# Optimization experiments

Measured on AMD Instinct MI355X. Metric: run time of the kernel, lower is better.

Reference implementation:

```python
import jax, jax.numpy as jnp
import numpy as np

N_HEAD = 16
LN_EPS = 1e-5

def _layernorm(x, g, b):
    mu = jnp.mean(x, axis=-1, keepdims=True)
    var = jnp.mean(jnp.square(x - mu), axis=-1, keepdims=True)
    return (x - mu) * jax.lax.rsqrt(var + LN_EPS) * g + b

def setup_inputs() -> dict:
    key = jax.random.key(0)
    ks = jax.random.split(key, 8)
    B, T, C, L, V = 4, 512, 1024, 8, 32000
    s = 0.02
    return {
        "idx": jax.random.randint(ks[0], (B, T), 0, V, dtype=jnp.int32),
        "tok_emb": jax.random.normal(ks[1], (V, C), jnp.float32) * s,
        "pos_emb": jax.random.normal(ks[2], (T, C), jnp.float32) * s,
        "ln1_g": jnp.ones((L, C), jnp.float32),
        "ln1_b": jnp.zeros((L, C), jnp.float32),
        "attn_w": jax.random.normal(ks[3], (L, 3 * C, C), jnp.float32) * s,
        "proj_w": jax.random.normal(ks[4], (L, C, C), jnp.float32) * s,
        "ln2_g": jnp.ones((L, C), jnp.float32),
        "ln2_b": jnp.zeros((L, C), jnp.float32),
        "mlp_w1": jax.random.normal(ks[5], (L, 4 * C, C), jnp.float32) * s,
        "mlp_w2": jax.random.normal(ks[6], (L, C, 4 * C), jnp.float32) * s,
        "lnf_g": jnp.ones((C,), jnp.float32),
        "lnf_b": jnp.zeros((C,), jnp.float32),
        "head_w": jax.random.normal(ks[7], (V, C), jnp.float32) * s,
    }

def reference(idx, tok_emb, pos_emb, ln1_g, ln1_b, attn_w, proj_w,
              ln2_g, ln2_b, mlp_w1, mlp_w2, lnf_g, lnf_b, head_w):
    B, T = idx.shape
    C = tok_emb.shape[1]
    H = N_HEAD
    D = C // H
    scale = 1.0 / np.sqrt(D).astype(np.float32)
    x = tok_emb[idx] + pos_emb[:T]            # [B,T,C]
    causal = jnp.tril(jnp.ones((T, T), bool))  # [T,T]

    def block(x, p):
        g1, b1, wqkv, wp, g2, b2, w1, w2 = p
        h = _layernorm(x, g1, b1)
        qkv = h @ wqkv.T                       # [B,T,3C]
        q, k, v = jnp.split(qkv, 3, axis=-1)
        q = q.reshape(B, T, H, D).transpose(0, 2, 1, 3)  # [B,H,T,D]
        k = k.reshape(B, T, H, D).transpose(0, 2, 1, 3)
        v = v.reshape(B, T, H, D).transpose(0, 2, 1, 3)
        att = jnp.einsum('bhqd,bhkd->bhqk', q, k) * scale
        att = jnp.where(causal, att, -jnp.inf)
        att = jax.nn.softmax(att, axis=-1)
        y = jnp.einsum('bhqk,bhkd->bhqd', att, v)
        y = y.transpose(0, 2, 1, 3).reshape(B, T, C)
        a = x + y @ wp.T                       # attn residual (inner)
        m = jax.nn.gelu(_layernorm(a, g2, b2) @ w1.T, approximate=False) @ w2.T
        # NOTE: faithful to source: outer residual adds x, not a
        return x + m, None

    x, _ = jax.lax.scan(block, x, (ln1_g, ln1_b, attn_w, proj_w,
                                   ln2_g, ln2_b, mlp_w1, mlp_w2))
    x = _layernorm(x, lnf_g, lnf_b)
    logits = x @ head_w.T                      # [B,T,V]
    return logits
```

## Files before the change

### kernel.cpp

```cpp
#include <hip/hip_runtime.h>
#include <stdint.h>

typedef unsigned short u16;
typedef __bf16 bf16_t;
typedef bf16_t bf16x8 __attribute__((ext_vector_type(8)));
typedef float f32x4 __attribute__((ext_vector_type(4)));

static __device__ __forceinline__ u16 f2bf(float f) {
  union { float f; uint32_t u; } cv; cv.f = f;
  uint32_t u = cv.u;
  return (u16)((u + 0x7FFFu + ((u >> 16) & 1u)) >> 16);
}

static __device__ __forceinline__ void gload16(const void* g, void* l) {
  __builtin_amdgcn_global_load_lds(
      (__attribute__((address_space(1))) void*)g,
      (__attribute__((address_space(3))) void*)l, 16, 0, 0);
}

__global__ __launch_bounds__(256) void embed_kernel(const int* __restrict__ idx,
                                                    const float* __restrict__ tok,
                                                    const float* __restrict__ pos,
                                                    float* __restrict__ x) {
  int row = blockIdx.x, tid = threadIdx.x;
  int t = row & 511;
  int v = idx[row];
  float4 a = ((const float4*)(tok + (long)v * 1024))[tid];
  float4 p = ((const float4*)(pos + (long)t * 1024))[tid];
  a.x += p.x; a.y += p.y; a.z += p.z; a.w += p.w;
  ((float4*)(x + (long)row * 1024))[tid] = a;
}

__global__ __launch_bounds__(256) void ln_kernel(const float* __restrict__ in,
                                                 const float* __restrict__ g,
                                                 const float* __restrict__ b,
                                                 u16* __restrict__ out) {
  int row = blockIdx.x, tid = threadIdx.x;
  int wid = tid >> 6, lane = tid & 63;
  const float4 v = ((const float4*)(in + (long)row * 1024))[tid];
  float s1 = v.x + v.y + v.z + v.w;
  float s2 = v.x*v.x + v.y*v.y + v.z*v.z + v.w*v.w;
#pragma unroll
  for (int o = 32; o >= 1; o >>= 1) { s1 += __shfl_xor(s1, o); s2 += __shfl_xor(s2, o); }
  __shared__ float red1[4], red2[4];
  if (lane == 0) { red1[wid] = s1; red2[wid] = s2; }
  __syncthreads();
  s1 = red1[0] + red1[1] + red1[2] + red1[3];
  s2 = red2[0] + red2[1] + red2[2] + red2[3];
  float mu = s1 * (1.f/1024.f);
  float var = s2 * (1.f/1024.f) - mu*mu;
  float rstd = rsqrtf(var + 1e-5f);
  const float4 gg = ((const float4*)g)[tid];
  const float4 bb = ((const float4*)b)[tid];
  ushort4 o4;
  o4.x = f2bf((v.x - mu)*rstd*gg.x + bb.x);
  o4.y = f2bf((v.y - mu)*rstd*gg.y + bb.y);
  o4.z = f2bf((v.z - mu)*rstd*gg.z + bb.z);
  o4.w = f2bf((v.w - mu)*rstd*gg.w + bb.w);
  ((ushort4*)(out + (long)row * 1024))[tid] = o4;
}

__global__ __launch_bounds__(256) void cast_kernel(const float* __restrict__ src,
                                                   u16* __restrict__ dst, int n4) {
  int i = blockIdx.x * 256 + threadIdx.x;
  if (i >= n4) return;
  float4 v = ((const float4*)src)[i];
  ushort4 o; o.x = f2bf(v.x); o.y = f2bf(v.y); o.z = f2bf(v.z); o.w = f2bf(v.w);
  ((ushort4*)dst)[i] = o;
}

__global__ __launch_bounds__(256) void cast4_kernel(const float* __restrict__ s0,
                                                    const float* __restrict__ s1,
                                                    const float* __restrict__ s2,
                                                    const float* __restrict__ s3,
                                                    u16* __restrict__ d0, u16* __restrict__ d1,
                                                    u16* __restrict__ d2, u16* __restrict__ d3) {
  int i = blockIdx.x * 256 + threadIdx.x;
  const float* s; u16* d; int off;
  if (i < 786432)       { s = s0; d = d0; off = i; }
  else if (i < 1048576) { s = s1; d = d1; off = i - 786432; }
  else if (i < 2097152) { s = s2; d = d2; off = i - 1048576; }
  else                  { s = s3; d = d3; off = i - 2097152; }
  float4 v = ((const float4*)s)[off];
  ushort4 o; o.x = f2bf(v.x); o.y = f2bf(v.y); o.z = f2bf(v.z); o.w = f2bf(v.w);
  ((ushort4*)d)[off] = o;
}

__global__ __launch_bounds__(256, 2) void qk_softmax_kernel(
    const u16* __restrict__ Q, const u16* __restrict__ Kt, u16* __restrict__ P) {
  constexpr int BK = 32;
  __shared__ __align__(16) u16 As[64 * BK];
  __shared__ __align__(16) u16 Bs[512 * BK];
  __shared__ float redmx[2][64], redsm[2][64];
  const int tid = threadIdx.x;
  const int wid = tid >> 6, lane = tid & 63;
  const int lm = lane & 15, lq = lane >> 4;
  const int wm = wid & 1, wn = wid >> 1;
  const int m0 = blockIdx.x * 64;
  const long z = blockIdx.z;
  const u16* Ab = Q + z * 32768;
  const u16* Bb = Kt + z * 32768;

  f32x4 acc[2][16];
  f32x4 zero = {0.f, 0.f, 0.f, 0.f};
#pragma unroll
  for (int i = 0; i < 2; ++i)
#pragma unroll
    for (int j = 0; j < 16; ++j) acc[i][j] = zero;

  const int fA = wid * 64 + lane;
  const u16* gA = Ab + (long)(m0 + (fA >> 2)) * 64 + ((fA & 3) << 3);
  u16* lA = &As[wid * 512];
  const u16* gB[8]; u16* lB[8];
#pragma unroll
  for (int i = 0; i < 8; ++i) {
    int f = (wid * 8 + i) * 64 + lane;
    gB[i] = Bb + (long)(f >> 2) * 64 + ((f & 3) << 3);
    lB[i] = &Bs[(wid * 8 + i) * 512];
  }

#pragma unroll
  for (int k0 = 0; k0 < 64; k0 += BK) {
    __syncthreads();
    gload16(gA + k0, lA);
#pragma unroll
    for (int i = 0; i < 8; ++i) gload16(gB[i] + k0, lB[i]);
    __syncthreads();
    bf16x8 af0 = *(const bf16x8*)&As[(wm * 32 + 0 * 16 + lm) * BK + lq * 8];
    bf16x8 af1 = *(const bf16x8*)&As[(wm * 32 + 1 * 16 + lm) * BK + lq * 8];
#pragma unroll
    for (int j = 0; j < 16; ++j) {
      bf16x8 bfr = *(const bf16x8*)&Bs[(wn * 256 + j * 16 + lm) * BK + lq * 8];
      acc[0][j] = __builtin_amdgcn_mfma_f32_16x16x32_bf16(af0, bfr, acc[0][j], 0, 0, 0);
      acc[1][j] = __builtin_amdgcn_mfma_f32_16x16x32_bf16(af1, bfr, acc[1][j], 0, 0, 0);
    }
  }

  float mx[2][4];
#pragma unroll
  for (int i = 0; i < 2; ++i)
#pragma unroll
    for (int r = 0; r < 4; ++r) {
      int q = m0 + wm * 32 + i * 16 + lq * 4 + r;
      float m = -3.4e38f;
#pragma unroll
      for (int j = 0; j < 16; ++j) {
        int col = wn * 256 + j * 16 + lm;
        float v = (col <= q) ? acc[i][j][r] * 0.125f : -3.4e38f;
        acc[i][j][r] = v;
        m = fmaxf(m, v);
      }
#pragma unroll
      for (int o = 8; o >= 1; o >>= 1) m = fmaxf(m, __shfl_xor(m, o));
      mx[i][r] = m;
    }
  if (lm == 0) {
#pragma unroll
    for (int i = 0; i < 2; ++i)
#pragma unroll
      for (int r = 0; r < 4; ++r)
        redmx[wn][wm * 32 + i * 16 + lq * 4 + r] = mx[i][r];
  }
  __syncthreads();

  float sm[2][4];
#pragma unroll
  for (int i = 0; i < 2; ++i)
#pragma unroll
    for (int r = 0; r < 4; ++r) {
      int rowloc = wm * 32 + i * 16 + lq * 4 + r;
      float m = fmaxf(redmx[0][rowloc], redmx[1][rowloc]);
      float s = 0.f;
#pragma unroll
      for (int j = 0; j < 16; ++j) {
        float e = __expf(acc[i][j][r] - m);
        acc[i][j][r] = e;
        s += e;
      }
#pragma unroll
      for (int o = 8; o >= 1; o >>= 1) s += __shfl_xor(s, o);
      sm[i][r] = s;
    }
  if (lm == 0) {
#pragma unroll
    for (int i = 0; i < 2; ++i)
#pragma unroll
      for (int r = 0; r < 4; ++r)
        redsm[wn][wm * 32 + i * 16 + lq * 4 + r] = sm[i][r];
  }
  __syncthreads();

  const int wlim = (m0 & ~127) + 128;
#pragma unroll
  for (int i = 0; i < 2; ++i)
#pragma unroll
    for (int r = 0; r < 4; ++r) {
      int rowloc = wm * 32 + i * 16 + lq * 4 + r;
      float inv = 1.f / (redsm[0][rowloc] + redsm[1][rowloc]);
      u16* prow = P + z * 262144 + (long)(m0 + rowloc) * 512;
#pragma unroll
      for (int j = 0; j < 16; ++j) {
        int col = wn * 256 + j * 16 + lm;
        if (col < wlim) prow[col] = f2bf(acc[i][j][r] * inv);
      }
    }
}

enum { EPI_F32 = 0, EPI_BF16 = 1, EPI_RES = 2, EPI_GELU = 3, EPI_QKV = 4 };

template<int BN, int EPI, bool CKLIM, bool XSWAP>
__global__ __launch_bounds__(256, 2) void gemm_nt(
    const u16* __restrict__ A, const u16* __restrict__ Bw,
    float* __restrict__ Cf, u16* __restrict__ Cb, const float* __restrict__ Res,
    int K, int ldc, float scale,
    long sAz, long sBz, long sCb, long sCh, int Hdiv,
    u16* __restrict__ q_out, u16* __restrict__ k_out, u16* __restrict__ vt_out) {
  constexpr int BM = 128, BK = 32;
  __shared__ __align__(16) u16 As[BM * BK];
  __shared__ __align__(16) u16 Bs[BN * BK];
  const int tid = threadIdx.x;
  const int wid = tid >> 6, lane = tid & 63;
  int mb, nb;
  if (XSWAP) {
    unsigned p = blockIdx.x + (blockIdx.y << 4);
    unsigned chunk = (gridDim.x * gridDim.y) >> 3;
    unsigned lg = (p & 7u) * chunk + (p >> 3);
    mb = (int)(lg & 15u); nb = (int)(lg >> 4);
  } else { nb = blockIdx.x; mb = blockIdx.y; }
  const int n0 = nb * BN, m0 = mb * BM;
  const long z = blockIdx.z;
  const u16* Ab = A + z * sAz;
  const u16* Bb = Bw + z * sBz;
  int kend = K;
  if (CKLIM) { int ke = m0 + BM; kend = ke < K ? ke : K; }

  const int wm = wid & 1, wn = wid >> 1;
  constexpr int NF = BN / 32;
  constexpr int BPW = BN / 64;
  f32x4 acc[4][NF];
  f32x4 zero = {0.f, 0.f, 0.f, 0.f};
#pragma unroll
  for (int i = 0; i < 4; ++i)
#pragma unroll
    for (int j = 0; j < NF; ++j) acc[i][j] = zero;

  const int fA0 = (wid * 2) * 64 + lane, fA1 = fA0 + 64;
  const u16* gA0 = Ab + (long)(m0 + (fA0 >> 2)) * K + ((fA0 & 3) << 3);
  const u16* gA1 = Ab + (long)(m0 + (fA1 >> 2)) * K + ((fA1 & 3) << 3);
  u16* lA0 = &As[(wid * 2) * 512];
  u16* lA1 = lA0 + 512;
  const u16* gB[BPW]; u16* lB[BPW];
#pragma unroll
  for (int i = 0; i < BPW; ++i) {
    int f = (wid * BPW + i) * 64 + lane;
    gB[i] = Bb + (long)(n0 + (f >> 2)) * K + ((f & 3) << 3);
    lB[i] = &Bs[(wid * BPW + i) * 512];
  }
  const int lm = lane & 15, lq = lane >> 4;

  for (int k0 = 0; k0 < kend; k0 += BK) {
    __syncthreads();
    gload16(gA0 + k0, lA0);
    gload16(gA1 + k0, lA1);
#pragma unroll
    for (int i = 0; i < BPW; ++i) gload16(gB[i] + k0, lB[i]);
    __syncthreads();
    bf16x8 af[4], bfr[NF];
#pragma unroll
    for (int i = 0; i < 4; ++i)
      af[i] = *(const bf16x8*)&As[(wm * 64 + i * 16 + lm) * BK + lq * 8];
#pragma unroll
    for (int j = 0; j < NF; ++j)
      bfr[j] = *(const bf16x8*)&Bs[(wn * (BN / 2) + j * 16 + lm) * BK + lq * 8];
#pragma unroll
    for (int i = 0; i < 4; ++i)
#pragma unroll
      for (int j = 0; j < NF; ++j)
        acc[i][j] = __builtin_amdgcn_mfma_f32_16x16x32_bf16(af[i], bfr[j], acc[i][j], 0, 0, 0);
  }

  const long coff = (z / Hdiv) * sCb + (z % Hdiv) * sCh;
#pragma unroll
  for (int i = 0; i < 4; ++i) {
#pragma unroll
    for (int j = 0; j < NF; ++j) {
#pragma unroll
      for (int r = 0; r < 4; ++r) {
        int row = m0 + wm * 64 + i * 16 + lq * 4 + r;
        int col = n0 + wn * (BN / 2) + j * 16 + lm;
        float v = acc[i][j][r];
        if (EPI == EPI_F32) {
          Cf[coff + (long)row * ldc + col] = v * scale;
        } else if (EPI == EPI_BF16) {
          Cb[coff + (long)row * ldc + col] = f2bf(v);
        } else if (EPI == EPI_RES) {
          long idx = (long)row * ldc + col;
          Cf[idx] = Res[idx] + v;
        } else if (EPI == EPI_GELU) {
          float gl = 0.5f * v * (1.0f + erff(v * 0.70710678118654752f));
          Cb[(long)row * ldc + col] = f2bf(gl);
        } else {
          int which = col >> 10, wc = col & 1023;
          int hh = wc >> 6, d = wc & 63;
          int bb2 = row >> 9, t = row & 511;
          long bh = bb2 * 16 + hh;
          u16 val = f2bf(v);
          if (which == 0)      q_out[(bh * 512 + t) * 64 + d] = val;
          else if (which == 1) k_out[(bh * 512 + t) * 64 + d] = val;
          else                 vt_out[(bh * 64 + d) * 512 + t] = val;
        }
      }
    }
  }
}

extern "C" void kernel_launch(void* const* d_in, const int* in_sizes, int n_in,
                              void* d_out, int out_size, void* d_ws, size_t ws_size,
                              hipStream_t stream) {
  (void)in_sizes; (void)n_in; (void)out_size; (void)ws_size;
  const int*   idx   = (const int*)  d_in[0];
  const float* tok   = (const float*)d_in[1];
  const float* pos   = (const float*)d_in[2];
  const float* ln1g  = (const float*)d_in[3];
  const float* ln1b  = (const float*)d_in[4];
  const float* attnw = (const float*)d_in[5];
  const float* projw = (const float*)d_in[6];
  const float* ln2g  = (const float*)d_in[7];
  const float* ln2b  = (const float*)d_in[8];
  const float* w1w   = (const float*)d_in[9];
  const float* w2w   = (const float*)d_in[10];
  const float* lnfg  = (const float*)d_in[11];
  const float* lnfb  = (const float*)d_in[12];
  const float* headw = (const float*)d_in[13];

  char* ob = (char*)d_out;
  u16*   Pb  = (u16*)  (ob + 67108864);
  u16*   m1b = (u16*)  (ob + 100663296);
  u16*   Qb  = (u16*)  (ob + 117440512);
  u16*   Kb  = (u16*)  (ob + 121634816);
  u16*   Vtb = (u16*)  (ob + 125829120);
  u16*   yb  = (u16*)  (ob + 130023424);
  float* ab  = (float*)(ob + 134217728);
  float* xb  = (float*)(ob + 142606336);

  char* wsb = (char*)d_ws;
  u16* hb    = (u16*)(wsb + 0);
  u16* wqkvb = (u16*)(wsb + 4194304);
  u16* wpb   = (u16*)(wsb + 10485760);
  u16* w1b   = (u16*)(wsb + 12582912);
  u16* w2b   = (u16*)(wsb + 20971520);
  u16* headb = (u16*)(wsb + 29360128);

  embed_kernel<<<2048, 256, 0, stream>>>(idx, tok, pos, xb);

  for (int l = 0; l < 8; ++l) {
    cast4_kernel<<<12288, 256, 0, stream>>>(
        attnw + (size_t)l * 3145728, projw + (size_t)l * 1048576,
        w1w + (size_t)l * 4194304,   w2w + (size_t)l * 4194304,
        wqkvb, wpb, w1b, w2b);
    ln_kernel<<<2048, 256, 0, stream>>>(xb, ln1g + l * 1024, ln1b + l * 1024, hb);
    gemm_nt<128, EPI_QKV, false, true><<<dim3(16, 24, 1), 256, 0, stream>>>(
        hb, wqkvb, nullptr, nullptr, nullptr, 1024, 0, 1.f,
        0, 0, 0, 0, 1, Qb, Kb, Vtb);
    qk_softmax_kernel<<<dim3(8, 1, 64), 256, 0, stream>>>(Qb, Kb, Pb);
    gemm_nt<64, EPI_BF16, true, false><<<dim3(1, 4, 64), 256, 0, stream>>>(
        Pb, Vtb, nullptr, yb, nullptr, 512, 1024, 1.f,
        262144, 32768, 524288, 64, 16, nullptr, nullptr, nullptr);
    gemm_nt<64, EPI_RES, false, true><<<dim3(16, 16, 1), 256, 0, stream>>>(
        yb, wpb, ab, nullptr, xb, 1024, 1024, 1.f,
        0, 0, 0, 0, 1, nullptr, nullptr, nullptr);
    ln_kernel<<<2048, 256, 0, stream>>>(ab, ln2g + l * 1024, ln2b + l * 1024, hb);
    gemm_nt<128, EPI_GELU, false, true><<<dim3(16, 32, 1), 256, 0, stream>>>(
        hb, w1b, nullptr, m1b, nullptr, 1024, 4096, 1.f,
        0, 0, 0, 0, 1, nullptr, nullptr, nullptr);
    gemm_nt<64, EPI_RES, false, true><<<dim3(16, 16, 1), 256, 0, stream>>>(
        m1b, w2b, xb, nullptr, xb, 4096, 1024, 1.f,
        0, 0, 0, 0, 1, nullptr, nullptr, nullptr);
  }

  ln_kernel<<<2048, 256, 0, stream>>>(xb, lnfg, lnfb, hb);
  cast_kernel<<<32000, 256, 0, stream>>>(headw, headb, 8192000);
  gemm_nt<128, EPI_F32, false, true><<<dim3(16, 250, 1), 256, 0, stream>>>(
      hb, headb, (float*)d_out, nullptr, nullptr, 1024, 32000, 1.f,
      0, 0, 0, 0, 1, nullptr, nullptr, nullptr);
}
```

Measured before the change: 2.393 ms.

## Add dedicated 256x256-tile pipelined LM-head GEMM kernel

Replaces the generic 128-tile GEMM for the vocabulary projection with a specialized 512-thread kernel that computes 256x256 output tiles. It double-buffers A and B in LDS through direct global-to-LDS loads, interleaves quarter-tile MFMA groups with prefetches under explicit barriers and waitcnts, raises wave priority around the MFMA groups, and remaps block indices so blocks sharing weight tiles run close together. The goal is more reuse per loaded byte and better overlap of loads with compute on the largest GEMM. In exchange it uses 128KB of LDS per block, hardcodes the shapes, and stores fp32 outputs element by element.

```diff
diff --git a/kernel.cpp b/kernel.cpp
--- a/kernel.cpp
+++ b/kernel.cpp
@@ -314,6 +314,142 @@
   }
 }
 
+__global__ __launch_bounds__(512, 2) void head_gemm256(
+    const u16* __restrict__ A, const u16* __restrict__ Bw, float* __restrict__ C) {
+  __shared__ __align__(16) u16 As[2 * 16384];
+  __shared__ __align__(16) u16 Bs[2 * 16384];
+  const int tid = threadIdx.x;
+  const int lane = tid & 63, wid = tid >> 6;
+  const int wm = wid >> 2, wn = wid & 3;
+  const int lm = lane & 15, lq = lane >> 4;
+
+  unsigned p = blockIdx.x;
+  unsigned lg = (p & 7u) * 125u + (p >> 3);
+  const long m0 = (long)(lg & 7u) << 8;
+  const long n0 = (long)(lg >> 3) << 8;
+
+  const int rS = tid >> 3, c8 = (tid & 7) << 3;
+  const u16* Ag = A + (m0 + rS) * 1024 + c8;
+  const u16* Bg = Bw + (n0 + rS) * 1024 + c8;
+  u16* lA = &As[rS * 64 + c8];
+  u16* lB = &Bs[rS * 64 + c8];
+
+#define STG_A(b, h, kt) do { \
+    gload16(Ag + (h)*131072 + (kt)*64,         lA + (b)*16384 + (h)*8192); \
+    gload16(Ag + (h)*131072 + 65536 + (kt)*64, lA + (b)*16384 + (h)*8192 + 4096); } while (0)
+#define STG_B(b, h, kt) do { \
+    gload16(Bg + (h)*131072 + (kt)*64,         lB + (b)*16384 + (h)*8192); \
+    gload16(Bg + (h)*131072 + 65536 + (kt)*64, lB + (b)*16384 + (h)*8192 + 4096); } while (0)
+
+  const u16* aRd = &As[(wm * 128 + lm) * 64 + lq * 8];
+  const u16* bRd = &Bs[(wn * 64 + lm) * 64 + lq * 8];
+#define ARD(b, mi, ks) (*(const bf16x8*)(aRd + (b)*16384 + (mi)*1024 + (ks)*32))
+#define BRD(b, nj, ks) (*(const bf16x8*)(bRd + (b)*16384 + (nj)*1024 + (ks)*32))
+#define BAR() __builtin_amdgcn_s_barrier()
+#define LGKM0() asm volatile("s_waitcnt lgkmcnt(0)")
+#define PRIO1() __builtin_amdgcn_s_setprio(1)
+#define PRIO0() __builtin_amdgcn_s_setprio(0)
+#define MMA_Q(AF, BF, MO, NO) \
+  _Pragma("unroll") for (int mi = 0; mi < 4; ++mi) \
+  _Pragma("unroll") for (int nj = 0; nj < 2; ++nj) { \
+    acc[mi+MO][nj+NO] = __builtin_amdgcn_mfma_f32_16x16x32_bf16(AF[mi][0], BF[nj][0], acc[mi+MO][nj+NO], 0, 0, 0); \
+    acc[mi+MO][nj+NO] = __builtin_amdgcn_mfma_f32_16x16x32_bf16(AF[mi][1], BF[nj][1], acc[mi+MO][nj+NO], 0, 0, 0); }
+
+  f32x4 acc[8][4];
+  f32x4 zero = {0.f, 0.f, 0.f, 0.f};
+#pragma unroll
+  for (int mi = 0; mi < 8; ++mi)
+#pragma unroll
+    for (int nj = 0; nj < 4; ++nj) acc[mi][nj] = zero;
+
+  STG_A(0, 0, 0); STG_A(0, 1, 0); STG_B(0, 0, 0); STG_B(0, 1, 0);
+  STG_B(1, 0, 1); STG_B(1, 1, 1);
+  asm volatile("s_waitcnt vmcnt(4)");
+  BAR();
+
+  bf16x8 a0[4][2], a1[4][2], b0[2][2], b1[2][2];
+
+#pragma unroll 1
+  for (int i = 0; i < 8; ++i) {
+    const int kt1 = 2 * i + 1;
+    const int ktn = 2 * i + 2;
+    const bool pf = (i < 7);
+#pragma unroll
+    for (int mi = 0; mi < 4; ++mi) { a0[mi][0] = ARD(0, mi, 0); a0[mi][1] = ARD(0, mi, 1); }
+#pragma unroll
+    for (int nj = 0; nj < 2; ++nj) { b0[nj][0] = BRD(0, nj, 0); b0[nj][1] = BRD(0, nj, 1); }
+    STG_A(1, 0, kt1);
+    BAR(); LGKM0(); PRIO1();
+    MMA_Q(a0, b0, 0, 0);
+    PRIO0(); BAR();
+#pragma unroll
+    for (int nj = 0; nj < 2; ++nj) { b1[nj][0] = BRD(0, nj + 2, 0); b1[nj][1] = BRD(0, nj + 2, 1); }
+    STG_A(1, 1, kt1);
+    BAR(); LGKM0(); PRIO1();
+    MMA_Q(a0, b1, 0, 2);
+    PRIO0(); BAR();
+#pragma unroll
+    for (int mi = 0; mi < 4; ++mi) { a1[mi][0] = ARD(0, mi + 4, 0); a1[mi][1] = ARD(0, mi + 4, 1); }
+    if (pf) STG_B(0, 0, ktn);
+    BAR(); LGKM0(); PRIO1();
+    MMA_Q(a1, b0, 4, 0);
+    PRIO0(); BAR();
+    if (pf) STG_B(0, 1, ktn);
+    if (i == 7) { asm volatile("s_waitcnt vmcnt(0)"); }
+    else        { asm volatile("s_waitcnt vmcnt(4)"); }
+    BAR(); PRIO1();
+    MMA_Q(a1, b1, 4, 2);
+    PRIO0(); BAR();
+#pragma unroll
+    for (int mi = 0; mi < 4; ++mi) { a0[mi][0] = ARD(1, mi, 0); a0[mi][1] = ARD(1, mi, 1); }
+#pragma unroll
+    for (int nj = 0; nj < 2; ++nj) { b0[nj][0] = BRD(1, nj, 0); b0[nj][1] = BRD(1, nj, 1); }
+    if (pf) STG_A(0, 0, ktn);
+    BAR(); LGKM0(); PRIO1();
+    MMA_Q(a0, b0, 0, 0);
+    PRIO0(); BAR();
+#pragma unroll
+    for (int nj = 0; nj < 2; ++nj) { b1[nj][0] = BRD(1, nj + 2, 0); b1[nj][1] = BRD(1, nj + 2, 1); }
+    if (pf) STG_A(0, 1, ktn);
+    BAR(); LGKM0(); PRIO1();
+    MMA_Q(a0, b1, 0, 2);
+    PRIO0(); BAR();
+#pragma unroll
+    for (int mi = 0; mi < 4; ++mi) { a1[mi][0] = ARD(1, mi + 4, 0); a1[mi][1] = ARD(1, mi + 4, 1); }
+    if (pf) STG_B(1, 0, kt1 + 2);
+    BAR(); LGKM0(); PRIO1();
+    MMA_Q(a1, b0, 4, 0);
+    PRIO0(); BAR();
+    if (pf) STG_B(1, 1, kt1 + 2);
+    asm volatile("s_waitcnt vmcnt(4)");
+    BAR(); PRIO1();
+    MMA_Q(a1, b1, 4, 2);
+    PRIO0(); BAR();
+  }
+
+#pragma unroll
+  for (int mi = 0; mi < 8; ++mi) {
+#pragma unroll
+    for (int nj = 0; nj < 4; ++nj) {
+#pragma unroll
+      for (int r = 0; r < 4; ++r) {
+        long row = m0 + wm * 128 + mi * 16 + lq * 4 + r;
+        long col = n0 + wn * 64 + nj * 16 + lm;
+        C[row * 32000 + col] = acc[mi][nj][r];
+      }
+    }
+  }
+#undef STG_A
+#undef STG_B
+#undef ARD
+#undef BRD
+#undef BAR
+#undef LGKM0
+#undef PRIO1
+#undef PRIO0
+#undef MMA_Q
+}
+
 extern "C" void kernel_launch(void* const* d_in, const int* in_sizes, int n_in,
                               void* d_out, int out_size, void* d_ws, size_t ws_size,
                               hipStream_t stream) {
@@ -380,7 +516,5 @@
 
   ln_kernel<<<2048, 256, 0, stream>>>(xb, lnfg, lnfb, hb);
   cast_kernel<<<32000, 256, 0, stream>>>(headw, headb, 8192000);
-  gemm_nt<128, EPI_F32, false, true><<<dim3(16, 250, 1), 256, 0, stream>>>(
-      hb, headb, (float*)d_out, nullptr, nullptr, 1024, 32000, 1.f,
-      0, 0, 0, 0, 1, nullptr, nullptr, nullptr);
-}
+  head_gemm256<<<1000, 512, 0, stream>>>(hb, headb, (float*)d_out);
+}
```

Result: no change. 2.427 ms (+1.4%).
